# Kernel tuning notes

Measured on AMD Instinct MI355X. Metric: run time of the kernel, lower is better.

The kernel has to match this reference:

```python
import jax, jax.numpy as jnp
import numpy as np


def setup_inputs() -> dict:
    key = jax.random.key(0)
    k1, k2, k3, k4, k5 = jax.random.split(key, 5)
    B, D, H, W, C = 2, 16, 16, 16, 256
    x = jax.random.normal(k1, (B, D, H, W, C), dtype=jnp.float32)
    Wf = jax.random.normal(k2, (C, C // 4), dtype=jnp.float32) * (1.0 / np.sqrt(C))
    Wg = jax.random.normal(k3, (C, C // 4), dtype=jnp.float32) * (1.0 / np.sqrt(C))
    Wh = jax.random.normal(k4, (C, C), dtype=jnp.float32) * (1.0 / np.sqrt(C))
    gamma = jax.random.normal(k5, (1,), dtype=jnp.float32) * 0.1
    return {"x": x, "Wf": Wf, "Wg": Wg, "Wh": Wh, "gamma": gamma}


def reference(x, Wf, Wg, Wh, gamma):
    B, D, H, W, C = x.shape
    N = D * H * W
    xf = x.reshape(B, N, C)  # hw_flatten of input (1x1x1 conv == per-position matmul)
    f = jnp.einsum('bnc,cf->bnf', xf, Wf)   # [B, N, C//4]
    g = jnp.einsum('bnc,cf->bnf', xf, Wg)   # [B, N, C//4]
    h = jnp.einsum('bnc,cf->bnf', xf, Wh)   # [B, N, C]
    s = jnp.einsum('bnf,bmf->bnm', g, f)    # g @ f^T, [B, N, N]
    beta = jax.nn.softmax(s, axis=-1)
    o = jnp.einsum('bnm,bmc->bnc', beta, h)  # [B, N, C]
    out = gamma * o.reshape(B, D, H, W, C) + x
    beta_out = beta.reshape(-1, D, H, W, 1)  # [B*N, D, H, W, 1] as in original
    return (out, beta_out)
```

## Files before the change

kernel.cpp:

```cpp
#include <hip/hip_runtime.h>

#define NPOS 4096
#define CDIM 256
#define FDIM 64

typedef short short8 __attribute__((ext_vector_type(8)));
typedef float f32x4 __attribute__((ext_vector_type(4)));

__device__ __forceinline__ unsigned short f2bf(float v) {
  unsigned u = __float_as_uint(v);
  unsigned r = (u + 0x7fffu + ((u >> 16) & 1u)) >> 16;
  return (unsigned short)r;
}
__device__ __forceinline__ float bf2f(unsigned short u) {
  return __uint_as_float((unsigned)u << 16);
}
__device__ __forceinline__ short8 as_s8(uint4 u) {
  return *reinterpret_cast<short8*>(&u);
}
__device__ __forceinline__ void gload_lds16(const void* g, void* l) {
  __builtin_amdgcn_global_load_lds(
      (const __attribute__((address_space(1))) unsigned int*)g,
      (__attribute__((address_space(3))) unsigned int*)l, 16, 0, 0);
}

__global__ __launch_bounds__(256) void proj_kernel(
    const float* __restrict__ x, const float* __restrict__ Wf,
    const float* __restrict__ Wg, const float* __restrict__ Wh,
    unsigned short* __restrict__ f_hi, unsigned short* __restrict__ f_lo,
    unsigned short* __restrict__ g_hi, unsigned short* __restrict__ g_lo,
    unsigned short* __restrict__ h_t) {
  __shared__ float xs[16][CDIM];
  const int row0 = blockIdx.x * 16;
  const int t = threadIdx.x;
  {
    const float4* xv = reinterpret_cast<const float4*>(x + (size_t)row0 * CDIM);
    float4* sv = reinterpret_cast<float4*>(&xs[0][0]);
#pragma unroll
    for (int i = 0; i < 4; ++i) sv[t + 256 * i] = xv[t + 256 * i];
  }
  __syncthreads();
  {
    float acc[16];
#pragma unroll
    for (int r = 0; r < 16; ++r) acc[r] = 0.f;
    for (int k = 0; k < CDIM; k += 4) {
      const float w0 = Wh[(size_t)(k + 0) * CDIM + t];
      const float w1 = Wh[(size_t)(k + 1) * CDIM + t];
      const float w2 = Wh[(size_t)(k + 2) * CDIM + t];
      const float w3 = Wh[(size_t)(k + 3) * CDIM + t];
#pragma unroll
      for (int r = 0; r < 16; ++r) {
        const float4 xv = *reinterpret_cast<const float4*>(&xs[r][k]);
        float a = acc[r];
        a = fmaf(xv.x, w0, a);
        a = fmaf(xv.y, w1, a);
        a = fmaf(xv.z, w2, a);
        a = fmaf(xv.w, w3, a);
        acc[r] = a;
      }
    }
    const int b = row0 >> 12;
    const int lr = row0 & (NPOS - 1);
    unsigned wd[8];
#pragma unroll
    for (int i = 0; i < 8; ++i)
      wd[i] = (unsigned)f2bf(acc[2 * i]) | ((unsigned)f2bf(acc[2 * i + 1]) << 16);
    uint4* base = reinterpret_cast<uint4*>(h_t + ((size_t)(b * CDIM + t)) * NPOS);
    const int m = t & 7;
    const int c0 = lr >> 3;
    base[c0 ^ m] = make_uint4(wd[0], wd[1], wd[2], wd[3]);
    base[(c0 + 1) ^ m] = make_uint4(wd[4], wd[5], wd[6], wd[7]);
  }
  {
    const int col = t & 63;
    const int rb = (t >> 6) * 4;
    const int colq = col >> 3, cwi = col & 7;
    float af[4] = {0.f, 0.f, 0.f, 0.f};
    float ag[4] = {0.f, 0.f, 0.f, 0.f};
    for (int k = 0; k < CDIM; k += 4) {
      const float wf0 = Wf[(size_t)(k + 0) * FDIM + col];
      const float wf1 = Wf[(size_t)(k + 1) * FDIM + col];
      const float wf2 = Wf[(size_t)(k + 2) * FDIM + col];
      const float wf3 = Wf[(size_t)(k + 3) * FDIM + col];
      const float wg0 = Wg[(size_t)(k + 0) * FDIM + col];
      const float wg1 = Wg[(size_t)(k + 1) * FDIM + col];
      const float wg2 = Wg[(size_t)(k + 2) * FDIM + col];
      const float wg3 = Wg[(size_t)(k + 3) * FDIM + col];
#pragma unroll
      for (int r = 0; r < 4; ++r) {
        const float4 xv = *reinterpret_cast<const float4*>(&xs[rb + r][k]);
        float a = af[r], bb = ag[r];
        a = fmaf(xv.x, wf0, a); a = fmaf(xv.y, wf1, a);
        a = fmaf(xv.z, wf2, a); a = fmaf(xv.w, wf3, a);
        bb = fmaf(xv.x, wg0, bb); bb = fmaf(xv.y, wg1, bb);
        bb = fmaf(xv.z, wg2, bb); bb = fmaf(xv.w, wg3, bb);
        af[r] = a; ag[r] = bb;
      }
    }
#pragma unroll
    for (int r = 0; r < 4; ++r) {
      const int row = row0 + rb + r;
      const int ph = ((colq ^ (row & 7)) << 3) | cwi;
      const size_t of = (size_t)row * FDIM + ph;
      const size_t og = (size_t)row * FDIM + col;
      const unsigned short fh = f2bf(af[r]);
      const unsigned short gh = f2bf(ag[r]);
      f_hi[of] = fh;
      f_lo[of] = f2bf(af[r] - bf2f(fh));
      g_hi[og] = gh;
      g_lo[og] = f2bf(ag[r] - bf2f(gh));
    }
  }
}

__global__ __launch_bounds__(512, 4) void qk_mfma_kernel(
    const unsigned short* __restrict__ f_hi, const unsigned short* __restrict__ f_lo,
    const unsigned short* __restrict__ g_hi, const unsigned short* __restrict__ g_lo,
    float* __restrict__ beta, float* __restrict__ lrow) {
  __shared__ uint4 Fh[2][128][8];
  __shared__ uint4 Fl[2][128][8];
  __shared__ float partl[8][16];

  const int wg = blockIdx.x;
  const int wgid = (wg & 7) * 64 + (wg >> 3);
  const int b = wgid >> 8;
  const int row0 = (wgid & 255) * 16;
  const int t = threadIdx.x;
  const int w = t >> 6;
  const int l = t & 63;
  const int lr = l & 15;
  const int lk = l >> 4;

  short8 gh[2], gl[2];
  {
    const unsigned short* gH = g_hi + ((size_t)(b * NPOS + row0 + lr)) * FDIM + lk * 8;
    const unsigned short* gL = g_lo + ((size_t)(b * NPOS + row0 + lr)) * FDIM + lk * 8;
#pragma unroll
    for (int ks = 0; ks < 2; ++ks) {
      gh[ks] = *reinterpret_cast<const short8*>(gH + ks * 32);
      gl[ks] = *reinterpret_cast<const short8*>(gL + ks * 32);
    }
  }

  const unsigned short* fbh = f_hi + (size_t)b * NPOS * FDIM;
  const unsigned short* fbl = f_lo + (size_t)b * NPOS * FDIM;

  float lsum = 0.f;
  unsigned short* Pb = (unsigned short*)(beta + (size_t)b * NPOS * NPOS);
  unsigned short* prow = Pb + (size_t)(row0 + lr) * (2 * NPOS) + NPOS;
  const int rsw = lr & 7;

#define STAGE(buf, tile)                                                       \
  do {                                                                         \
    const int tile0_ = (tile) * 128;                                           \
    _Pragma("unroll")                                                          \
    for (int j = 0; j < 2; ++j) {                                              \
      const int slot_ = j * 512 + t;                                           \
      const int row_ = slot_ >> 3, ch_ = slot_ & 7;                            \
      gload_lds16(fbh + (size_t)(tile0_ + row_) * FDIM + ch_ * 8,              \
                  (unsigned short*)&Fh[buf][0][0] + (size_t)slot_ * 8);        \
      gload_lds16(fbl + (size_t)(tile0_ + row_) * FDIM + ch_ * 8,              \
                  (unsigned short*)&Fl[buf][0][0] + (size_t)slot_ * 8);        \
    }                                                                          \
  } while (0)

  STAGE(0, 0);
  __syncthreads();

  const int rrA = w * 16 + lr;
  const int fsw = rrA & 7;
  int buf = 0;
  for (int tile = 0; tile < 32; ++tile) {
    if (tile < 31) STAGE(buf ^ 1, tile + 1);
    const uint4 h0 = Fh[buf][rrA][lk ^ fsw];
    const uint4 h1 = Fh[buf][rrA][(lk + 4) ^ fsw];
    const uint4 q0 = Fl[buf][rrA][lk ^ fsw];
    const uint4 q1 = Fl[buf][rrA][(lk + 4) ^ fsw];
    f32x4 acca = {0.f, 0.f, 0.f, 0.f};
    f32x4 accb = {0.f, 0.f, 0.f, 0.f};
    acca = __builtin_amdgcn_mfma_f32_16x16x32_bf16(as_s8(h0), gh[0], acca, 0, 0, 0);
    accb = __builtin_amdgcn_mfma_f32_16x16x32_bf16(as_s8(h0), gl[0], accb, 0, 0, 0);
    acca = __builtin_amdgcn_mfma_f32_16x16x32_bf16(as_s8(q0), gh[0], acca, 0, 0, 0);
    accb = __builtin_amdgcn_mfma_f32_16x16x32_bf16(as_s8(h1), gh[1], accb, 0, 0, 0);
    acca = __builtin_amdgcn_mfma_f32_16x16x32_bf16(as_s8(q1), gh[1], acca, 0, 0, 0);
    accb = __builtin_amdgcn_mfma_f32_16x16x32_bf16(as_s8(h1), gl[1], accb, 0, 0, 0);
    const f32x4 acc = acca + accb;
    const int cq = tile * 128 + w * 16 + lk * 4;
    const float e0 = __expf(acc[0]);
    const float e1 = __expf(acc[1]);
    const float e2 = __expf(acc[2]);
    const float e3 = __expf(acc[3]);
    lsum += (e0 + e1) + (e2 + e3);
    uint2 pk;
    pk.x = (unsigned)f2bf(e0) | ((unsigned)f2bf(e1) << 16);
    pk.y = (unsigned)f2bf(e2) | ((unsigned)f2bf(e3) << 16);
    const int sidx = (((cq >> 3) ^ rsw) << 3) | (cq & 7);
    *reinterpret_cast<uint2*>(prow + sidx) = pk;
    __syncthreads();
    buf ^= 1;
  }
#undef STAGE

  lsum += __shfl_xor(lsum, 16);
  lsum += __shfl_xor(lsum, 32);
  if (l < 16) partl[w][l] = lsum;
  __syncthreads();
  if (t < 16) {
    float s = 0.f;
#pragma unroll
    for (int q = 0; q < 8; ++q) s += partl[q][t];
    lrow[(size_t)b * NPOS + row0 + t] = s;
  }
}

__global__ __launch_bounds__(1024, 4) void pv_gemm_kernel(
    const unsigned short* __restrict__ h_t, const float* __restrict__ x,
    const float* __restrict__ lrow, const float* __restrict__ gamma,
    float* __restrict__ beta, float* __restrict__ out) {
  __shared__ uint4 Ab[2][32][8];
  __shared__ uint4 Bb[2][256][8];
  __shared__ float linvs[32];

  const int wg = blockIdx.x;
  const int wgid = (wg & 7) * 32 + (wg >> 3);
  const int b = wgid >> 7;
  const int row0 = (wgid & 127) * 32;
  const int t = threadIdx.x;
  const int w = t >> 6;
  const int l = t & 63;
  const int wr = w & 1;
  const int wc = w >> 1;

  if (t < 32) linvs[t] = __frcp_rn(lrow[(size_t)b * NPOS + row0 + t]);

  const size_t hoff = (size_t)b * CDIM * NPOS;
  const unsigned short* Pub = (const unsigned short*)(beta + (size_t)b * NPOS * NPOS);

#define STAGE(buf, kt)                                                          \
  do {                                                                          \
    {                                                                           \
      const int slot_ = w * 128 + l;                                            \
      const unsigned short* g_ = h_t + hoff + (size_t)(slot_ >> 3) * NPOS +     \
                                 (size_t)((kt) * 8 + (slot_ & 7)) * 8;          \
      gload_lds16(g_, (unsigned short*)&Bb[buf][0][0] + (size_t)(w * 128) * 8); \
    }                                                                           \
    {                                                                           \
      const int slot_ = w * 128 + 64 + l;                                       \
      const unsigned short* g_ = h_t + hoff + (size_t)(slot_ >> 3) * NPOS +     \
                                 (size_t)((kt) * 8 + (slot_ & 7)) * 8;          \
      gload_lds16(g_, (unsigned short*)&Bb[buf][0][0] +                         \
                          (size_t)(w * 128 + 64) * 8);                          \
    }                                                                           \
    if (t < 256) {                                                              \
      const unsigned short* g_ = Pub + (size_t)(row0 + (t >> 3)) * (2 * NPOS) + \
                                 NPOS + (size_t)((kt) * 8 + (t & 7)) * 8;       \
      gload_lds16(g_, (unsigned short*)&Ab[buf][0][0] + (size_t)(w * 64) * 8);  \
    }                                                                           \
  } while (0)

  f32x4 acc0 = {0.f, 0.f, 0.f, 0.f}, acc1 = {0.f, 0.f, 0.f, 0.f};
  const int ar = wr * 16 + (l & 15);
  const int lk = l >> 4;
  const int c0 = wc * 32 + (l & 15);
  const int c1 = c0 + 16;
  const int brow = t >> 5;
  const int jj = t & 31;

  STAGE(0, 0);
  __syncthreads();

  int buf = 0;
  for (int kt = 0; kt < 64; ++kt) {
    if (kt < 63) STAGE(buf ^ 1, kt + 1);
    {
      const uint4 a0 = Ab[buf][ar][lk ^ (ar & 7)];
      const uint4 a1 = Ab[buf][ar][(4 + lk) ^ (ar & 7)];
      const uint4 b00 = Bb[buf][c0][lk ^ (c0 & 7)];
      const uint4 b01 = Bb[buf][c1][lk ^ (c1 & 7)];
      const uint4 b10 = Bb[buf][c0][(4 + lk) ^ (c0 & 7)];
      const uint4 b11 = Bb[buf][c1][(4 + lk) ^ (c1 & 7)];
      acc0 = __builtin_amdgcn_mfma_f32_16x16x32_bf16(as_s8(a0), as_s8(b00), acc0, 0, 0, 0);
      acc1 = __builtin_amdgcn_mfma_f32_16x16x32_bf16(as_s8(a0), as_s8(b01), acc1, 0, 0, 0);
      acc0 = __builtin_amdgcn_mfma_f32_16x16x32_bf16(as_s8(a1), as_s8(b10), acc0, 0, 0, 0);
      acc1 = __builtin_amdgcn_mfma_f32_16x16x32_bf16(as_s8(a1), as_s8(b11), acc1, 0, 0, 0);
    }
    {
      const float il = linvs[brow];
      const unsigned* arow = reinterpret_cast<const unsigned*>(&Ab[buf][brow][0]);
      const unsigned u = arow[(((jj >> 2) ^ (brow & 7)) << 2) | (jj & 3)];
      float2 v;
      v.x = bf2f((unsigned short)(u & 0xffffu)) * il;
      v.y = bf2f((unsigned short)(u >> 16)) * il;
      *reinterpret_cast<float2*>(beta + (size_t)(b * NPOS + row0 + brow) * NPOS +
                                 (size_t)kt * 64 + jj * 2) = v;
    }
    __syncthreads();
    buf ^= 1;
  }
#undef STAGE

  const float gam = gamma[0];
#pragma unroll
  for (int r = 0; r < 4; ++r) {
    const int lrr = wr * 16 + (l >> 4) * 4 + r;
    const int orow = row0 + lrr;
    const float sc = gam * linvs[lrr];
    const size_t i0 = ((size_t)b * NPOS + orow) * CDIM + wc * 32 + (l & 15);
    out[i0] = fmaf(sc, acc0[r], x[i0]);
    out[i0 + 16] = fmaf(sc, acc1[r], x[i0 + 16]);
  }
}

extern "C" void kernel_launch(void* const* d_in, const int* in_sizes, int n_in,
                              void* d_out, int out_size, void* d_ws, size_t ws_size,
                              hipStream_t stream) {
  (void)in_sizes; (void)n_in; (void)out_size; (void)ws_size;
  const float* x = (const float*)d_in[0];
  const float* Wf = (const float*)d_in[1];
  const float* Wg = (const float*)d_in[2];
  const float* Wh = (const float*)d_in[3];
  const float* gamma = (const float*)d_in[4];

  float* out = (float*)d_out;
  float* beta = out + (size_t)2 * NPOS * CDIM;

  unsigned short* h_t = (unsigned short*)d_ws;
  unsigned short* f_hi = h_t + (size_t)2 * CDIM * NPOS;
  unsigned short* f_lo = f_hi + (size_t)2 * NPOS * FDIM;
  unsigned short* g_hi = f_lo + (size_t)2 * NPOS * FDIM;
  unsigned short* g_lo = g_hi + (size_t)2 * NPOS * FDIM;
  float* lrow = (float*)(g_lo + (size_t)2 * NPOS * FDIM);

  hipLaunchKernelGGL(proj_kernel, dim3(2 * NPOS / 16), dim3(256), 0, stream,
                     x, Wf, Wg, Wh, f_hi, f_lo, g_hi, g_lo, h_t);
  hipLaunchKernelGGL(qk_mfma_kernel, dim3(512), dim3(512), 0, stream,
                     f_hi, f_lo, g_hi, g_lo, beta, lrow);
  hipLaunchKernelGGL(pv_gemm_kernel, dim3(256), dim3(1024), 0, stream,
                     h_t, x, lrow, gamma, beta, out);
}
```

Before: 136.6 us.

## Fuse QK softmax-exp and PV GEMM kernels into one attention kernel

Merges the QK^T/exp kernel and the PV GEMM kernel into a single 1024-thread kernel in which each workgroup handles 32 query rows. The row sums stay in LDS instead of going through a global lrow buffer, and one kernel launch is removed. __syncthreads is replaced with explicit s_waitcnt vmcnt(1)/s_barrier asm so the next tile's prefetch can stay in flight across the barrier. The grid halves to 256 workgroups for the QK phase, which reduces parallelism. The LDS buffers are aliased between phases, which depends on the barrier ordering being correct.

```diff
diff --git a/kernel.cpp b/kernel.cpp
--- a/kernel.cpp
+++ b/kernel.cpp
@@ -114,65 +114,69 @@
   }
 }
 
-__global__ __launch_bounds__(512, 4) void qk_mfma_kernel(
+__global__ __launch_bounds__(1024, 4) void attn_fused_kernel(
     const unsigned short* __restrict__ f_hi, const unsigned short* __restrict__ f_lo,
     const unsigned short* __restrict__ g_hi, const unsigned short* __restrict__ g_lo,
-    float* __restrict__ beta, float* __restrict__ lrow) {
-  __shared__ uint4 Fh[2][128][8];
-  __shared__ uint4 Fl[2][128][8];
-  __shared__ float partl[8][16];
+    const unsigned short* __restrict__ h_t, const float* __restrict__ x,
+    const float* __restrict__ gamma, float* __restrict__ beta,
+    float* __restrict__ out) {
+  __shared__ __align__(16) char shraw[73728];
+  __shared__ float partl[16][16];
+  __shared__ float linvs[32];
+  uint4 (*Fh)[128][8] = reinterpret_cast<uint4(*)[128][8]>(shraw);
+  uint4 (*Fl)[128][8] = reinterpret_cast<uint4(*)[128][8]>(shraw + 32768);
+  uint4 (*Ab)[32][8] = reinterpret_cast<uint4(*)[32][8]>(shraw);
+  uint4 (*Bb)[256][8] = reinterpret_cast<uint4(*)[256][8]>(shraw + 8192);
 
   const int wg = blockIdx.x;
-  const int wgid = (wg & 7) * 64 + (wg >> 3);
-  const int b = wgid >> 8;
-  const int row0 = (wgid & 255) * 16;
+  const int wgid = (wg & 7) * 32 + (wg >> 3);
+  const int b = wgid >> 7;
+  const int row0 = (wgid & 127) * 32;
   const int t = threadIdx.x;
   const int w = t >> 6;
   const int l = t & 63;
   const int lr = l & 15;
   const int lk = l >> 4;
 
+  const int wr = w >> 3;
+  const int wq = w & 7;
+  const int arow = row0 + wr * 16 + lr;
   short8 gh[2], gl[2];
   {
-    const unsigned short* gH = g_hi + ((size_t)(b * NPOS + row0 + lr)) * FDIM + lk * 8;
-    const unsigned short* gL = g_lo + ((size_t)(b * NPOS + row0 + lr)) * FDIM + lk * 8;
+    const unsigned short* gH = g_hi + ((size_t)(b * NPOS + arow)) * FDIM + lk * 8;
+    const unsigned short* gL = g_lo + ((size_t)(b * NPOS + arow)) * FDIM + lk * 8;
 #pragma unroll
     for (int ks = 0; ks < 2; ++ks) {
       gh[ks] = *reinterpret_cast<const short8*>(gH + ks * 32);
       gl[ks] = *reinterpret_cast<const short8*>(gL + ks * 32);
     }
   }
-
   const unsigned short* fbh = f_hi + (size_t)b * NPOS * FDIM;
   const unsigned short* fbl = f_lo + (size_t)b * NPOS * FDIM;
-
+  unsigned short* Pb = (unsigned short*)(beta + (size_t)b * NPOS * NPOS);
+  unsigned short* prow = Pb + (size_t)arow * (2 * NPOS) + NPOS;
+  const int rsw = lr & 7;
   float lsum = 0.f;
-  unsigned short* Pb = (unsigned short*)(beta + (size_t)b * NPOS * NPOS);
-  unsigned short* prow = Pb + (size_t)(row0 + lr) * (2 * NPOS) + NPOS;
-  const int rsw = lr & 7;
-
-#define STAGE(buf, tile)                                                       \
+  const int srow_ = t >> 3, sch_ = t & 7;
+
+#define STAGEA(buf, tile)                                                      \
   do {                                                                         \
-    const int tile0_ = (tile) * 128;                                           \
-    _Pragma("unroll")                                                          \
-    for (int j = 0; j < 2; ++j) {                                              \
-      const int slot_ = j * 512 + t;                                           \
-      const int row_ = slot_ >> 3, ch_ = slot_ & 7;                            \
-      gload_lds16(fbh + (size_t)(tile0_ + row_) * FDIM + ch_ * 8,              \
-                  (unsigned short*)&Fh[buf][0][0] + (size_t)slot_ * 8);        \
-      gload_lds16(fbl + (size_t)(tile0_ + row_) * FDIM + ch_ * 8,              \
-                  (unsigned short*)&Fl[buf][0][0] + (size_t)slot_ * 8);        \
-    }                                                                          \
+    const int tr_ = (tile) * 128 + srow_;                                      \
+    gload_lds16(fbh + (size_t)tr_ * FDIM + sch_ * 8,                           \
+                (char*)&Fh[buf][0][0] + (size_t)t * 16);                       \
+    gload_lds16(fbl + (size_t)tr_ * FDIM + sch_ * 8,                           \
+                (char*)&Fl[buf][0][0] + (size_t)t * 16);                       \
   } while (0)
 
-  STAGE(0, 0);
-  __syncthreads();
-
-  const int rrA = w * 16 + lr;
+  STAGEA(0, 0);
+  asm volatile("s_waitcnt vmcnt(0) lgkmcnt(0)\ns_barrier" ::: "memory");
+
+  const int rrA = wq * 16 + lr;
   const int fsw = rrA & 7;
   int buf = 0;
   for (int tile = 0; tile < 32; ++tile) {
-    if (tile < 31) STAGE(buf ^ 1, tile + 1);
+    if (tile < 31) STAGEA(buf ^ 1, tile + 1);
+    __builtin_amdgcn_sched_barrier(0);
     const uint4 h0 = Fh[buf][rrA][lk ^ fsw];
     const uint4 h1 = Fh[buf][rrA][(lk + 4) ^ fsw];
     const uint4 q0 = Fl[buf][rrA][lk ^ fsw];
@@ -186,7 +190,7 @@
     acca = __builtin_amdgcn_mfma_f32_16x16x32_bf16(as_s8(q1), gh[1], acca, 0, 0, 0);
     accb = __builtin_amdgcn_mfma_f32_16x16x32_bf16(as_s8(h1), gl[1], accb, 0, 0, 0);
     const f32x4 acc = acca + accb;
-    const int cq = tile * 128 + w * 16 + lk * 4;
+    const int cq = tile * 128 + wq * 16 + lk * 4;
     const float e0 = __expf(acc[0]);
     const float e1 = __expf(acc[1]);
     const float e2 = __expf(acc[2]);
@@ -197,47 +201,28 @@
     pk.y = (unsigned)f2bf(e2) | ((unsigned)f2bf(e3) << 16);
     const int sidx = (((cq >> 3) ^ rsw) << 3) | (cq & 7);
     *reinterpret_cast<uint2*>(prow + sidx) = pk;
-    __syncthreads();
+    asm volatile("s_waitcnt vmcnt(1) lgkmcnt(0)\ns_barrier" ::: "memory");
     buf ^= 1;
   }
-#undef STAGE
+#undef STAGEA
 
   lsum += __shfl_xor(lsum, 16);
   lsum += __shfl_xor(lsum, 32);
   if (l < 16) partl[w][l] = lsum;
   __syncthreads();
-  if (t < 16) {
+  if (t < 32) {
+    const int half = t >> 4;
     float s = 0.f;
 #pragma unroll
-    for (int q = 0; q < 8; ++q) s += partl[q][t];
-    lrow[(size_t)b * NPOS + row0 + t] = s;
-  }
-}
-
-__global__ __launch_bounds__(1024, 4) void pv_gemm_kernel(
-    const unsigned short* __restrict__ h_t, const float* __restrict__ x,
-    const float* __restrict__ lrow, const float* __restrict__ gamma,
-    float* __restrict__ beta, float* __restrict__ out) {
-  __shared__ uint4 Ab[2][32][8];
-  __shared__ uint4 Bb[2][256][8];
-  __shared__ float linvs[32];
-
-  const int wg = blockIdx.x;
-  const int wgid = (wg & 7) * 32 + (wg >> 3);
-  const int b = wgid >> 7;
-  const int row0 = (wgid & 127) * 32;
-  const int t = threadIdx.x;
-  const int w = t >> 6;
-  const int l = t & 63;
-  const int wr = w & 1;
-  const int wc = w >> 1;
-
-  if (t < 32) linvs[t] = __frcp_rn(lrow[(size_t)b * NPOS + row0 + t]);
+    for (int q = 0; q < 8; ++q) s += partl[half * 8 + q][t & 15];
+    linvs[t] = __frcp_rn(s);
+  }
+  asm volatile("s_waitcnt vmcnt(0) lgkmcnt(0)\ns_barrier" ::: "memory");
 
   const size_t hoff = (size_t)b * CDIM * NPOS;
   const unsigned short* Pub = (const unsigned short*)(beta + (size_t)b * NPOS * NPOS);
 
-#define STAGE(buf, kt)                                                          \
+#define STAGEB(buf, kt)                                                         \
   do {                                                                          \
     {                                                                           \
       const int slot_ = w * 128 + l;                                            \
@@ -260,22 +245,24 @@
   } while (0)
 
   f32x4 acc0 = {0.f, 0.f, 0.f, 0.f}, acc1 = {0.f, 0.f, 0.f, 0.f};
-  const int ar = wr * 16 + (l & 15);
-  const int lk = l >> 4;
-  const int c0 = wc * 32 + (l & 15);
+  const int wrB = w & 1;
+  const int wcB = w >> 1;
+  const int arB = wrB * 16 + lr;
+  const int c0 = wcB * 32 + lr;
   const int c1 = c0 + 16;
   const int brow = t >> 5;
   const int jj = t & 31;
 
-  STAGE(0, 0);
-  __syncthreads();
-
-  int buf = 0;
+  STAGEB(0, 0);
+  asm volatile("s_waitcnt vmcnt(0) lgkmcnt(0)\ns_barrier" ::: "memory");
+
+  buf = 0;
   for (int kt = 0; kt < 64; ++kt) {
-    if (kt < 63) STAGE(buf ^ 1, kt + 1);
+    if (kt < 63) STAGEB(buf ^ 1, kt + 1);
+    __builtin_amdgcn_sched_barrier(0);
     {
-      const uint4 a0 = Ab[buf][ar][lk ^ (ar & 7)];
-      const uint4 a1 = Ab[buf][ar][(4 + lk) ^ (ar & 7)];
+      const uint4 a0 = Ab[buf][arB][lk ^ (arB & 7)];
+      const uint4 a1 = Ab[buf][arB][(4 + lk) ^ (arB & 7)];
       const uint4 b00 = Bb[buf][c0][lk ^ (c0 & 7)];
       const uint4 b01 = Bb[buf][c1][lk ^ (c1 & 7)];
       const uint4 b10 = Bb[buf][c0][(4 + lk) ^ (c0 & 7)];
@@ -287,26 +274,26 @@
     }
     {
       const float il = linvs[brow];
-      const unsigned* arow = reinterpret_cast<const unsigned*>(&Ab[buf][brow][0]);
-      const unsigned u = arow[(((jj >> 2) ^ (brow & 7)) << 2) | (jj & 3)];
+      const unsigned* arow_ = reinterpret_cast<const unsigned*>(&Ab[buf][brow][0]);
+      const unsigned u = arow_[(((jj >> 2) ^ (brow & 7)) << 2) | (jj & 3)];
       float2 v;
       v.x = bf2f((unsigned short)(u & 0xffffu)) * il;
       v.y = bf2f((unsigned short)(u >> 16)) * il;
       *reinterpret_cast<float2*>(beta + (size_t)(b * NPOS + row0 + brow) * NPOS +
                                  (size_t)kt * 64 + jj * 2) = v;
     }
-    __syncthreads();
+    asm volatile("s_waitcnt vmcnt(1) lgkmcnt(0)\ns_barrier" ::: "memory");
     buf ^= 1;
   }
-#undef STAGE
+#undef STAGEB
 
   const float gam = gamma[0];
 #pragma unroll
   for (int r = 0; r < 4; ++r) {
-    const int lrr = wr * 16 + (l >> 4) * 4 + r;
+    const int lrr = wrB * 16 + lk * 4 + r;
     const int orow = row0 + lrr;
     const float sc = gam * linvs[lrr];
-    const size_t i0 = ((size_t)b * NPOS + orow) * CDIM + wc * 32 + (l & 15);
+    const size_t i0 = ((size_t)b * NPOS + orow) * CDIM + wcB * 32 + lr;
     out[i0] = fmaf(sc, acc0[r], x[i0]);
     out[i0 + 16] = fmaf(sc, acc1[r], x[i0 + 16]);
   }
@@ -330,12 +317,9 @@
   unsigned short* f_lo = f_hi + (size_t)2 * NPOS * FDIM;
   unsigned short* g_hi = f_lo + (size_t)2 * NPOS * FDIM;
   unsigned short* g_lo = g_hi + (size_t)2 * NPOS * FDIM;
-  float* lrow = (float*)(g_lo + (size_t)2 * NPOS * FDIM);
 
   hipLaunchKernelGGL(proj_kernel, dim3(2 * NPOS / 16), dim3(256), 0, stream,
                      x, Wf, Wg, Wh, f_hi, f_lo, g_hi, g_lo, h_t);
-  hipLaunchKernelGGL(qk_mfma_kernel, dim3(512), dim3(512), 0, stream,
-                     f_hi, f_lo, g_hi, g_lo, beta, lrow);
-  hipLaunchKernelGGL(pv_gemm_kernel, dim3(256), dim3(1024), 0, stream,
-                     h_t, x, lrow, gamma, beta, out);
-}
+  hipLaunchKernelGGL(attn_fused_kernel, dim3(256), dim3(1024), 0, stream,
+                     f_hi, f_lo, g_hi, g_lo, h_t, x, gamma, beta, out);
+}
```

After: 133.0 us. 1.03x faster.
